# Optimization experiments

Measured on AMD Instinct MI355X. Metric: run time of the kernel, lower is better.

## Reference

```python
import jax, jax.numpy as jnp
import numpy as np

N = 50000   # nodes
E = 800000  # edges
B = 50      # graphs
EPS = 1e-5


def setup_inputs() -> dict:
    key = jax.random.key(0)
    ks = jax.random.split(key, 32)
    x = jax.random.normal(ks[0], (N, 128), dtype=jnp.float32)
    edge_index = jax.random.randint(ks[1], (2, E), 0, N, dtype=jnp.int32)
    batch = jnp.sort(jax.random.randint(ks[2], (N,), 0, B, dtype=jnp.int32))
    dims = [(128, 256), (256, 512), (512, 256), (256, 128)]
    inp = {"x": x, "edge_index": edge_index, "batch": batch}
    ki = 3
    for i, (cin, cout) in enumerate(dims, start=1):
        s = 1.0 / np.sqrt(cin)
        inp[f"conv{i}_W"] = jax.random.uniform(ks[ki], (3, cin, cout), jnp.float32, -s, s); ki += 1
        inp[f"conv{i}_b"] = jax.random.uniform(ks[ki], (cout,), jnp.float32, -s, s); ki += 1
        inp[f"gn{i}_w"] = jnp.ones((cout,), jnp.float32)
        inp[f"gn{i}_b"] = jnp.zeros((cout,), jnp.float32)
        inp[f"gn{i}_ms"] = jnp.ones((cout,), jnp.float32)
    inp["lin1_W"] = jax.random.uniform(ks[ki], (128, 64), jnp.float32, -1/np.sqrt(128), 1/np.sqrt(128)); ki += 1
    inp["lin1_b"] = jnp.zeros((64,), jnp.float32)
    inp["lin2_W"] = jax.random.uniform(ks[ki], (64, 10), jnp.float32, -1/np.sqrt(64), 1/np.sqrt(64)); ki += 1
    inp["lin2_b"] = jnp.zeros((10,), jnp.float32)
    return inp


def _cheb_conv(x, src, dst, nw, W, b):
    # PyG ChebConv, K=3, sym norm, lambda_max=2 => L_hat = -D^-1/2 A D^-1/2
    def prop(h):
        return jax.ops.segment_sum(nw[:, None] * h[src], dst, num_segments=N)
    Tx0 = x
    Tx1 = prop(x)
    Tx2 = 2.0 * prop(Tx1) - Tx0
    return Tx0 @ W[0] + Tx1 @ W[1] + Tx2 @ W[2] + b


def _graph_norm(x, batch, cnt, w, b, ms):
    mean = jax.ops.segment_sum(x, batch, num_segments=B) / cnt[:, None]
    sub = x - ms * mean[batch]
    var = jax.ops.segment_sum(sub * sub, batch, num_segments=B) / cnt[:, None]
    return w * sub * jax.lax.rsqrt(var[batch] + EPS) + b


def reference(x, edge_index, batch,
              conv1_W, conv1_b, gn1_w, gn1_b, gn1_ms,
              conv2_W, conv2_b, gn2_w, gn2_b, gn2_ms,
              conv3_W, conv3_b, gn3_w, gn3_b, gn3_ms,
              conv4_W, conv4_b, gn4_w, gn4_b, gn4_ms,
              lin1_W, lin1_b, lin2_W, lin2_b):
    src, dst = edge_index[0], edge_index[1]
    deg = jax.ops.segment_sum(jnp.ones((E,), x.dtype), dst, num_segments=N)
    dinv = jnp.where(deg > 0, jax.lax.rsqrt(jnp.maximum(deg, 1.0)), 0.0)
    nw = -dinv[src] * dinv[dst]  # scaled-Laplacian edge weights
    cnt = jnp.maximum(jax.ops.segment_sum(jnp.ones((N,), x.dtype), batch, num_segments=B), 1.0)

    h = x
    layers = [(conv1_W, conv1_b, gn1_w, gn1_b, gn1_ms),
              (conv2_W, conv2_b, gn2_w, gn2_b, gn2_ms),
              (conv3_W, conv3_b, gn3_w, gn3_b, gn3_ms),
              (conv4_W, conv4_b, gn4_w, gn4_b, gn4_ms)]
    for (W, bb, gw, gb, gms) in layers:
        h = _cheb_conv(h, src, dst, nw, W, bb)
        h = _graph_norm(h, batch, cnt, gw, gb, gms)
        h = jnp.where(h >= 0, h, 0.2 * h)  # leaky_relu(0.2)
    h = h + x  # residual
    pooled = jax.ops.segment_sum(h, batch, num_segments=B) / cnt[:, None]
    out = jnp.tanh(pooled @ lin1_W + lin1_b)
    return out @ lin2_W + lin2_b
```

## Files before the change

kernel.cpp:

```cpp
#include <hip/hip_runtime.h>

#define NN 50000
#define EE 800000
#define BG 50

typedef unsigned short ushort_t;
typedef __bf16 bf16x8 __attribute__((ext_vector_type(8)));
typedef float f32x4 __attribute__((ext_vector_type(4)));

__device__ __forceinline__ float b2f(ushort_t h) {
    unsigned int u = ((unsigned int)h) << 16;
    float f; __builtin_memcpy(&f, &u, 4); return f;
}
__device__ __forceinline__ ushort_t f2b(float f) {
    unsigned int u; __builtin_memcpy(&u, &f, 4);
    unsigned int r = u + 0x7fffu + ((u >> 16) & 1u);
    return (ushort_t)(r >> 16);
}

__device__ __forceinline__ void async_ld16(const void* g, void* l) {
    __builtin_amdgcn_global_load_lds(
        (__attribute__((address_space(1))) unsigned int*)(void*)g,
        (__attribute__((address_space(3))) unsigned int*)l, 16, 0, 0);
}

__global__ void k_detect(const ushort_t* xs, int* flag) {
    __shared__ int cnt;
    if (threadIdx.x == 0) cnt = 0;
    __syncthreads();
    int e = (xs[2 * threadIdx.x] >> 7) & 0xFF;
    if (e >= 96 && e <= 142) atomicAdd(&cnt, 1);
    __syncthreads();
    if (threadIdx.x == 0) *flag = (cnt >= 300) ? 1 : 0;
}

struct CastJobs {
    const void* src[25];
    int off[25];
    int start[26];
};
__global__ void k_castall(CastJobs jb, ushort_t* base, const int* flag, int total) {
    int i = blockIdx.x * 256 + threadIdx.x;
    if (i >= total) return;
    int lo = 0;
    while (i >= jb.start[lo + 1]) ++lo;
    int k = i - jb.start[lo];
    const void* s = jb.src[lo];
    ushort_t v;
    if (*flag) v = ((const ushort_t*)s)[k];
    else       v = f2b(((const float*)s)[k]);
    base[jb.off[lo] + k] = v;
}

__global__ void k_deg(const int* edge, int* degi) {
    int e = blockIdx.x * 256 + threadIdx.x;
    if (e < EE) atomicAdd(&degi[edge[EE + e]], 1);
}
__global__ void k_scan1(const int* degi, int* rowptr, int* bsum, float* dinv) {
    __shared__ int sh[1024];
    int t = threadIdx.x, i = blockIdx.x * 1024 + t;
    int v = (i < NN) ? degi[i] : 0;
    if (i < NN) dinv[i] = v > 0 ? rsqrtf((float)v) : 0.0f;
    sh[t] = v; __syncthreads();
    for (int off = 1; off < 1024; off <<= 1) {
        int add = (t >= off) ? sh[t - off] : 0;
        __syncthreads();
        sh[t] += add;
        __syncthreads();
    }
    if (i < NN) rowptr[i] = sh[t] - v;
    if (t == 1023) bsum[blockIdx.x] = sh[t];
}
__global__ void k_scan2(const int* bsum, int* boff, int* rowptr,
                        const int* batch, float* cntf) {
    int t = threadIdx.x;
    if (t == 0) {
        int run = 0;
        for (int j = 0; j < 49; ++j) { boff[j] = run; run += bsum[j]; }
        rowptr[NN] = run;
    }
    if (t < BG) {
        int g = t;
        int lo = 0, hi = NN;
        while (lo < hi) { int m = (lo + hi) >> 1; if (batch[m] < g) lo = m + 1; else hi = m; }
        int a = lo; lo = 0; hi = NN;
        while (lo < hi) { int m = (lo + hi) >> 1; if (batch[m] < g + 1) lo = m + 1; else hi = m; }
        cntf[g] = fmaxf((float)(lo - a), 1.0f);
    }
}
__global__ void k_scan3(int* rowptr, const int* boff) {
    int i = blockIdx.x * 256 + threadIdx.x;
    if (i < NN) rowptr[i] += boff[i >> 10];
}
__global__ void k_fill(const int* edge, const float* dinv, const int* rowptr,
                       int* cursor, int2* epack) {
    int e = blockIdx.x * 256 + threadIdx.x;
    if (e >= EE) return;
    int s = edge[e], d = edge[EE + e];
    int slot = atomicAdd(&cursor[d], 1);
    int pos = rowptr[d] + slot;
    float wv = -dinv[s] * dinv[d];
    int2 pk; pk.x = s; __builtin_memcpy(&pk.y, &wv, 4);
    epack[pos] = pk;
}

struct TJobs {
    int soff[8], doff[8], K[8], C[8];
    int tstart[9];
};
__global__ void k_transposeAll(TJobs tj, const ushort_t* Wst, ushort_t* WTall) {
    __shared__ ushort_t tile[32][33];
    int b = blockIdx.x;
    int j = 0;
    while (b >= tj.tstart[j + 1]) ++j;
    int t = b - tj.tstart[j];
    int K = tj.K[j], C = tj.C[j];
    int tilesX = K >> 5;
    int bx = (t % tilesX) * 32, by = (t / tilesX) * 32;
    const ushort_t* W = Wst + tj.soff[j];
    ushort_t* WT = WTall + tj.doff[j];
    int tx = threadIdx.x, ty = threadIdx.y;
    for (int i = ty; i < 32; i += 8) tile[i][tx] = W[(size_t)(bx + i) * C + by + tx];
    __syncthreads();
    for (int i = ty; i < 32; i += 8) WT[(size_t)(by + i) * K + bx + tx] = tile[tx][i];
}

template<int SL>
__launch_bounds__(256)
__global__ void k_prop3(ushort_t* out, int ldo,
                        const ushort_t* src, int lds_, int soff,
                        const ushort_t* addP, int lda_, int aoff,
                        const ushort_t* subP, int ldsu, int suoff,
                        const ushort_t* bias, float alpha,
                        const int* rowptr, const int2* epack) {
    constexpr int EG = 64 / SL;
    int n = blockIdx.x * 4 + (threadIdx.x >> 6);
    if (n >= NN) return;
    int lane = threadIdx.x & 63;
    int eg = lane / SL;
    int cpos = (lane % SL) * 8;
    int r0 = rowptr[n], r1 = rowptr[n + 1];
    float acc[8];
#pragma unroll
    for (int i = 0; i < 8; ++i) acc[i] = 0.f;
    const ushort_t* sbase = src + soff + cpos;
    int j = r0 + eg;
    for (; j + 7 * EG < r1; j += 8 * EG) {
        int2 p[8];
#pragma unroll
        for (int u = 0; u < 8; ++u) p[u] = epack[j + u * EG];
        __bf16 v[8][8];
#pragma unroll
        for (int u = 0; u < 8; ++u)
            __builtin_memcpy(v[u], sbase + (size_t)p[u].x * lds_, 16);
#pragma unroll
        for (int u = 0; u < 8; ++u) {
            float wv; __builtin_memcpy(&wv, &p[u].y, 4);
#pragma unroll
            for (int i = 0; i < 8; ++i) acc[i] += wv * (float)v[u][i];
        }
    }
    for (; j + 3 * EG < r1; j += 4 * EG) {
        int2 p[4];
#pragma unroll
        for (int u = 0; u < 4; ++u) p[u] = epack[j + u * EG];
        __bf16 v[4][8];
#pragma unroll
        for (int u = 0; u < 4; ++u)
            __builtin_memcpy(v[u], sbase + (size_t)p[u].x * lds_, 16);
#pragma unroll
        for (int u = 0; u < 4; ++u) {
            float wv; __builtin_memcpy(&wv, &p[u].y, 4);
#pragma unroll
            for (int i = 0; i < 8; ++i) acc[i] += wv * (float)v[u][i];
        }
    }
    for (; j < r1; j += EG) {
        int2 p0 = epack[j];
        float wv; __builtin_memcpy(&wv, &p0.y, 4);
        __bf16 v0[8];
        __builtin_memcpy(v0, sbase + (size_t)p0.x * lds_, 16);
#pragma unroll
        for (int i = 0; i < 8; ++i) acc[i] += wv * (float)v0[i];
    }
#pragma unroll
    for (int off = SL; off < 64; off <<= 1)
#pragma unroll
        for (int i = 0; i < 8; ++i) acc[i] += __shfl_xor(acc[i], off);

    if (eg == 0) {
        float res[8];
#pragma unroll
        for (int i = 0; i < 8; ++i) res[i] = alpha * acc[i];
        if (addP) {
            __bf16 a[8];
            __builtin_memcpy(a, addP + (size_t)n * lda_ + aoff + cpos, 16);
#pragma unroll
            for (int i = 0; i < 8; ++i) res[i] += (float)a[i];
        }
        if (subP) {
            __bf16 sm[8];
            __builtin_memcpy(sm, subP + (size_t)n * ldsu + suoff + cpos, 16);
#pragma unroll
            for (int i = 0; i < 8; ++i) res[i] -= (float)sm[i];
        }
        if (bias) {
            __bf16 bb[8];
            __builtin_memcpy(bb, bias + cpos, 16);
#pragma unroll
            for (int i = 0; i < 8; ++i) res[i] += (float)bb[i];
        }
        ushort_t o[8];
#pragma unroll
        for (int i = 0; i < 8; ++i) o[i] = f2b(res[i]);
        __builtin_memcpy(out + (size_t)n * ldo + cpos, o, 16);
    }
}

__launch_bounds__(256)
__global__ void k_gemm(const ushort_t* A0, const ushort_t* A1, const ushort_t* A2,
                       int lda, const ushort_t* WT, const ushort_t* bias, int hasBias,
                       ushort_t* out, int ldout, int Ktot, int NX, int MT) {
    __shared__ __align__(16) ushort_t ldsA[128 * 64];
    __shared__ __align__(16) ushort_t ldsB[128 * 64];
    const int lin = blockIdx.x;
    const int x7 = lin & 7, rr = lin >> 3;
    const int n_t = rr % NX, mhi = rr / NX;
    const int m_t = mhi * 8 + x7;
    if (m_t >= MT) return;
    const int tid = threadIdx.x, lane = tid & 63, w = tid >> 6;
    const int wm = w & 1, wn = w >> 1;
    const int m0 = m_t * 128, n0 = n_t * 128;
    const int KT = Ktot / 64, per = lda >> 6;

    f32x4 acc[4][4];
#pragma unroll
    for (int i = 0; i < 4; ++i)
#pragma unroll
        for (int j = 0; j < 4; ++j) acc[i][j] = (f32x4){0.f, 0.f, 0.f, 0.f};

    const int srow = lane >> 3;
    const int scolX = (((lane & 7) ^ srow) << 3);
    const int l7 = lane & 7;

    for (int kt = 0; kt < KT; ++kt) {
        int seg = kt / per, lk = (kt - seg * per) * 64;
        const ushort_t* Ap = (seg == 0) ? A0 : ((seg == 1) ? A1 : A2);
        __syncthreads();
#pragma unroll
        for (int t = 0; t < 4; ++t) {
            int inst = (w << 2) + t;
            int row = inst * 8 + srow;
            int gr = m0 + row; if (gr >= NN) gr = NN - 1;
            async_ld16(Ap + (size_t)gr * lda + lk + scolX, &ldsA[inst * 512]);
            async_ld16(WT + (size_t)(n0 + row) * Ktot + kt * 64 + scolX, &ldsB[inst * 512]);
        }
        __builtin_amdgcn_s_waitcnt(0);
        __syncthreads();
#pragma unroll
        for (int kk = 0; kk < 64; kk += 32) {
            bf16x8 aF[4], bF[4];
            int qx = ((((kk >> 3) + (lane >> 4)) ^ l7) << 3);
#pragma unroll
            for (int i = 0; i < 4; ++i) {
                aF[i] = *(const bf16x8*)&ldsA[(wm * 64 + i * 16 + (lane & 15)) * 64 + qx];
                bF[i] = *(const bf16x8*)&ldsB[(wn * 64 + i * 16 + (lane & 15)) * 64 + qx];
            }
#pragma unroll
            for (int i = 0; i < 4; ++i)
#pragma unroll
                for (int j = 0; j < 4; ++j)
                    acc[i][j] = __builtin_amdgcn_mfma_f32_16x16x32_bf16(aF[i], bF[j], acc[i][j], 0, 0, 0);
        }
    }
#pragma unroll
    for (int i = 0; i < 4; ++i) {
        int rbase = m0 + wm * 64 + i * 16 + ((lane >> 4) << 2);
#pragma unroll
        for (int j = 0; j < 4; ++j) {
            int col = n0 + wn * 64 + j * 16 + (lane & 15);
            float bv = hasBias ? b2f(bias[col]) : 0.0f;
#pragma unroll
            for (int r = 0; r < 4; ++r) {
                int row = rbase + r;
                if (row < NN) out[(size_t)row * ldout + col] = f2b(acc[i][j][r] + bv);
            }
        }
    }
}

template<int VEC>
__launch_bounds__(256)
__global__ void k_stats2(const ushort_t* h, const int* batch, float* sums, float* sumsq,
                         int withSq) {
    constexpr int C = VEC * 64;
    int wave = threadIdx.x >> 6, lane = threadIdx.x & 63;
    int n0 = blockIdx.x * 128 + wave * 32;
    if (n0 >= NN) return;
    int n1 = n0 + 32 < NN ? n0 + 32 : NN;
    int coff = lane * VEC;
    float s[VEC], sq[VEC];
#pragma unroll
    for (int i = 0; i < VEC; ++i) { s[i] = 0.f; sq[i] = 0.f; }
    int cur = batch[n0];
    for (int n = n0; n < n1; ++n) {
        int g = batch[n];
        if (g != cur) {
#pragma unroll
            for (int i = 0; i < VEC; ++i) {
                atomicAdd(&sums[cur * C + coff + i], s[i]);
                if (withSq) atomicAdd(&sumsq[cur * C + coff + i], sq[i]);
                s[i] = 0.f; sq[i] = 0.f;
            }
            cur = g;
        }
        __bf16 v[VEC];
        __builtin_memcpy(v, h + (size_t)n * C + coff, VEC * 2);
#pragma unroll
        for (int i = 0; i < VEC; ++i) {
            float f = (float)v[i];
            s[i] += f; sq[i] += f * f;
        }
    }
#pragma unroll
    for (int i = 0; i < VEC; ++i) {
        atomicAdd(&sums[cur * C + coff + i], s[i]);
        if (withSq) atomicAdd(&sumsq[cur * C + coff + i], sq[i]);
    }
}

template<int VEC>
__launch_bounds__(256)
__global__ void k_norm2(const ushort_t* hpre, const int* batch, const float* sums,
                        const float* sumsq, const float* cntf,
                        const ushort_t* gw, const ushort_t* gb, const ushort_t* gms,
                        const ushort_t* xres, ushort_t* out, int addres) {
    constexpr int C = VEC * 64;
    int n = blockIdx.x * 4 + (threadIdx.x >> 6);
    if (n >= NN) return;
    int lane = threadIdx.x & 63;
    int coff = lane * VEC;
    int g = batch[n];
    float cg = cntf[g];
    float sm[VEC], sq[VEC];
    __builtin_memcpy(sm, sums  + g * C + coff, VEC * 4);
    __builtin_memcpy(sq, sumsq + g * C + coff, VEC * 4);
    __bf16 vgw[VEC], vgb[VEC], vms[VEC], vh[VEC];
    __builtin_memcpy(vgw, gw + coff, VEC * 2);
    __builtin_memcpy(vgb, gb + coff, VEC * 2);
    __builtin_memcpy(vms, gms + coff, VEC * 2);
    __builtin_memcpy(vh, hpre + (size_t)n * C + coff, VEC * 2);
    __bf16 vx[VEC];
    if (addres) __builtin_memcpy(vx, xres + (size_t)n * 128 + coff, VEC * 2);
    ushort_t o[VEC];
#pragma unroll
    for (int i = 0; i < VEC; ++i) {
        float mean = sm[i] / cg;
        float ms = (float)vms[i];
        float var = sq[i] / cg - mean * mean * ms * (2.0f - ms);
        var = fmaxf(var, 0.0f);
        float y = (float)vgw[i] * ((float)vh[i] - ms * mean) * rsqrtf(var + 1e-5f) + (float)vgb[i];
        y = (y >= 0.0f) ? y : 0.2f * y;
        if (addres) y += (float)vx[i];
        o[i] = f2b(y);
    }
    __builtin_memcpy(out + (size_t)n * C + coff, o, VEC * 2);
}

__global__ void k_head(const float* pooled, const float* cntf,
                       const ushort_t* W1, const ushort_t* b1,
                       const ushort_t* W2, const ushort_t* b2s, void* out,
                       const int* flag) {
    __shared__ float pl[128];
    __shared__ float hid[64];
    int g = blockIdx.x, t = threadIdx.x;
    float inv = 1.0f / cntf[g];
    for (int k = t; k < 128; k += 64) pl[k] = pooled[g * 128 + k] * inv;
    __syncthreads();
    float a = b2f(b1[t]);
    for (int k = 0; k < 128; ++k) a += pl[k] * b2f(W1[k * 64 + t]);
    hid[t] = tanhf(a);
    __syncthreads();
    if (t < 10) {
        float o = b2f(b2s[t]);
        for (int j = 0; j < 64; ++j) o += hid[j] * b2f(W2[j * 10 + t]);
        if (*flag) ((ushort_t*)out)[g * 10 + t] = f2b(o);
        else       ((float*)out)[g * 10 + t]    = o;
    }
}

extern "C" void kernel_launch(void* const* d_in, const int* in_sizes, int n_in,
                              void* d_out, int out_size, void* d_ws, size_t ws_size,
                              hipStream_t stream) {
    (void)in_sizes; (void)n_in; (void)out_size; (void)ws_size;

    const void* x_raw = d_in[0];
    const int* edge   = (const int*)d_in[1];
    const int* batch  = (const int*)d_in[2];

    char* ws = (char*)d_ws;
    float*    dinv   = (float*)   (ws + 0);
    int*      degi   = (int*)     (ws + 200192);
    int*      rowptr = (int*)     (ws + 400384);
    int*      cursor = (int*)     (ws + 600576);
    int*      bsum   = (int*)     (ws + 800768);
    int*      boff   = (int*)     (ws + 801024);
    float*    cntf   = (float*)   (ws + 801280);
    float*    sums   = (float*)   (ws + 801536);
    float*    sumsq  = (float*)   (ws + 903936);
    float*    pooled = (float*)   (ws + 1006336);
    int*      dflag  = (int*)     (ws + 1031936);
    ushort_t* Xb     = (ushort_t*)(ws + 1032192);
    ushort_t* Wst    = (ushort_t*)(ws + 13832192);
    ushort_t* WTall  = (ushort_t*)(ws + 15798272);
    ushort_t* SB     = (ushort_t*)(ws + 17764352);
    int2*     epack  = (int2*)    (ws + 17791488);
    ushort_t* T1     = (ushort_t*)(ws + 24191488);
    ushort_t* T2     = (ushort_t*)(ws + 75391488);
    ushort_t* P      = (ushort_t*)(ws + 126591488);
    ushort_t* HA     = (ushort_t*)(ws + 177791488);

    const int cins[4]  = {128, 256, 512, 256};
    const int couts[4] = {256, 512, 256, 128};
    const size_t wtoff[4] = {0, 98304, 491520, 884736};
    const int bo[4] = {0, 256, 768, 1024};
    const int gwo = 1152, gbo = 2304, gmo = 3456;
    const int l1Wo = 4608, l1bo = 12800, l2Wo = 12864, l2bo = 13504;

    const int XB_E = 1032192 / 2, WST_E = 13832192 / 2, SB_E = 17764352 / 2;

    CastJobs jb;
    int sizes[25]; int nj = 0;
    auto addjob = [&](const void* s, int off, int n) {
        jb.src[nj] = s; jb.off[nj] = off; sizes[nj] = n; ++nj;
    };
    addjob(x_raw, XB_E, NN * 128);
    for (int l = 0; l < 4; ++l) {
        addjob(d_in[3 + 5 * l], WST_E + (int)wtoff[l], 3 * cins[l] * couts[l]);
        addjob(d_in[4 + 5 * l], SB_E + bo[l],        couts[l]);
        addjob(d_in[5 + 5 * l], SB_E + gwo + bo[l],  couts[l]);
        addjob(d_in[6 + 5 * l], SB_E + gbo + bo[l],  couts[l]);
        addjob(d_in[7 + 5 * l], SB_E + gmo + bo[l],  couts[l]);
    }
    addjob(d_in[23], SB_E + l1Wo, 128 * 64);
    addjob(d_in[24], SB_E + l1bo, 64);
    addjob(d_in[25], SB_E + l2Wo, 64 * 10);
    addjob(d_in[26], SB_E + l2bo, 10);
    int run = 0;
    for (int k = 0; k < 25; ++k) { jb.start[k] = run; run += sizes[k]; }
    jb.start[25] = run;

    TJobs tj;
    int tn = 0, trun = 0;
    auto addt = [&](int soff, int doff, int K, int C) {
        tj.soff[tn] = soff; tj.doff[tn] = doff; tj.K[tn] = K; tj.C[tn] = C;
        tj.tstart[tn] = trun; trun += (K / 32) * (C / 32); ++tn;
    };
    addt((int)wtoff[0], (int)wtoff[0], 3 * cins[0], couts[0]);
    addt((int)wtoff[1], (int)wtoff[1], 3 * cins[1], couts[1]);
    for (int l = 2; l < 4; ++l)
        for (int j2 = 0; j2 < 3; ++j2) {
            int o = (int)wtoff[l] + j2 * cins[l] * couts[l];
            addt(o, o, cins[l], couts[l]);
        }
    tj.tstart[8] = trun;

    k_detect<<<1, 512, 0, stream>>>((const ushort_t*)x_raw, dflag);
    hipMemsetAsync(degi,   0, NN * 4, stream);
    hipMemsetAsync(cursor, 0, NN * 4, stream);
    hipMemsetAsync(pooled, 0, BG * 128 * 4, stream);

    k_castall<<<(run + 255) / 256, 256, 0, stream>>>(jb, (ushort_t*)ws, dflag, run);

    k_deg<<<(EE + 255) / 256, 256, 0, stream>>>(edge, degi);
    k_scan1<<<49, 1024, 0, stream>>>(degi, rowptr, bsum, dinv);
    k_scan2<<<1, 64, 0, stream>>>(bsum, boff, rowptr, batch, cntf);
    k_scan3<<<(NN + 255) / 256, 256, 0, stream>>>(rowptr, boff);
    k_fill<<<(EE + 255) / 256, 256, 0, stream>>>(edge, dinv, rowptr, cursor, epack);

    k_transposeAll<<<trun, dim3(32, 8), 0, stream>>>(tj, Wst, WTall);

    const int NB = (NN + 3) / 4;
    const int SBk = (NN + 127) / 128;
    const int MT = (NN + 127) / 128;
    const int MG = (MT + 7) / 8;
    auto prop = [&](int C, ushort_t* o, int ldo,
                    const ushort_t* s, int lds_, int soff,
                    const ushort_t* aP, int lda_, int aoff,
                    const ushort_t* sP, int ldsu, int suoff,
                    const ushort_t* bias, float alpha) {
        if (C == 128)
            k_prop3<16><<<NB, 256, 0, stream>>>(o, ldo, s, lds_, soff, aP, lda_, aoff,
                                                sP, ldsu, suoff, bias, alpha, rowptr, epack);
        else
            k_prop3<32><<<NB, 256, 0, stream>>>(o, ldo, s, lds_, soff, aP, lda_, aoff,
                                                sP, ldsu, suoff, bias, alpha, rowptr, epack);
    };
    auto gemm = [&](const ushort_t* A0, const ushort_t* A1, const ushort_t* A2,
                    int lda, const ushort_t* WT, const ushort_t* bias, int hasBias,
                    ushort_t* o, int ldout, int Ktot, int NX) {
        k_gemm<<<MG * 8 * NX, 256, 0, stream>>>(A0, A1, A2, lda, WT, bias, hasBias,
                                                o, ldout, Ktot, NX, MT);
    };
    auto stats = [&](int C, const ushort_t* h, float* sm, float* sq, int withSq) {
        if (C == 128)      k_stats2<2><<<SBk, 256, 0, stream>>>(h, batch, sm, sq, withSq);
        else if (C == 256) k_stats2<4><<<SBk, 256, 0, stream>>>(h, batch, sm, sq, withSq);
        else               k_stats2<8><<<SBk, 256, 0, stream>>>(h, batch, sm, sq, withSq);
    };
    auto norm = [&](int C, const ushort_t* hp, const ushort_t* gwp, const ushort_t* gbp,
                    const ushort_t* gmp, ushort_t* o, int addres) {
        if (C == 128)      k_norm2<2><<<NB, 256, 0, stream>>>(hp, batch, sums, sumsq, cntf, gwp, gbp, gmp, Xb, o, addres);
        else if (C == 256) k_norm2<4><<<NB, 256, 0, stream>>>(hp, batch, sums, sumsq, cntf, gwp, gbp, gmp, Xb, o, addres);
        else               k_norm2<8><<<NB, 256, 0, stream>>>(hp, batch, sums, sumsq, cntf, gwp, gbp, gmp, Xb, o, addres);
    };

    ushort_t* G = T1;
    const ushort_t* hin = Xb;
    for (int l = 0; l < 4; ++l) {
        int cin = cins[l], cout = couts[l];
        if (l < 2) {
            prop(cin, T1, cin, hin, cin, 0, nullptr, 0, 0, nullptr, 0, 0, nullptr, 1.0f);
            prop(cin, T2, cin, T1, cin, 0, nullptr, 0, 0, hin, cin, 0, nullptr, 2.0f);
            gemm(hin, T1, T2, cin, WTall + wtoff[l], SB + bo[l], 1, P, cout, 3 * cin,
                 cout / 128);
        } else {
            gemm(hin, hin, hin, cin, WTall + wtoff[l], nullptr, 0, G, 3 * cout, cin,
                 (3 * cout) / 128);
            ushort_t* V = HA;
            prop(cout, V, cout, G, 3 * cout, 2 * cout, G, 3 * cout, cout,
                 nullptr, 0, 0, nullptr, 2.0f);
            prop(cout, P, cout, V, cout, 0, G, 3 * cout, 0,
                 G, 3 * cout, 2 * cout, SB + bo[l], 1.0f);
        }
        hipMemsetAsync(sums, 0, 2 * 102400, stream);
        stats(cout, P, sums, sumsq, 1);
        norm(cout, P, SB + gwo + bo[l], SB + gbo + bo[l], SB + gmo + bo[l], HA, l == 3);
        hin = HA;
    }
    stats(128, HA, pooled, pooled, 0);
    k_head<<<BG, 64, 0, stream>>>(pooled, cntf, SB + l1Wo, SB + l1bo, SB + l2Wo, SB + l2bo,
                                  d_out, dflag);
}
```

Baseline: 1.109 ms.

## Compute graph stats per-graph block without atomics and drop memsets

Result: slower. 1.275 ms (+15.0%).

```diff
diff --git a/kernel.cpp b/kernel.cpp
--- a/kernel.cpp
+++ b/kernel.cpp
@@ -39,8 +39,10 @@
     int off[25];
     int start[26];
 };
-__global__ void k_castall(CastJobs jb, ushort_t* base, const int* flag, int total) {
+__global__ void k_castall(CastJobs jb, ushort_t* base, const int* flag, int total,
+                          int* degi) {
     int i = blockIdx.x * 256 + threadIdx.x;
+    if (i < NN) degi[i] = 0;
     if (i >= total) return;
     int lo = 0;
     while (i >= jb.start[lo + 1]) ++lo;
@@ -72,12 +74,13 @@
     if (t == 1023) bsum[blockIdx.x] = sh[t];
 }
 __global__ void k_scan2(const int* bsum, int* boff, int* rowptr,
-                        const int* batch, float* cntf) {
+                        const int* batch, float* cntf, int* gstart) {
     int t = threadIdx.x;
     if (t == 0) {
         int run = 0;
         for (int j = 0; j < 49; ++j) { boff[j] = run; run += bsum[j]; }
         rowptr[NN] = run;
+        gstart[BG] = NN;
     }
     if (t < BG) {
         int g = t;
@@ -85,12 +88,13 @@
         while (lo < hi) { int m = (lo + hi) >> 1; if (batch[m] < g) lo = m + 1; else hi = m; }
         int a = lo; lo = 0; hi = NN;
         while (lo < hi) { int m = (lo + hi) >> 1; if (batch[m] < g + 1) lo = m + 1; else hi = m; }
+        gstart[g] = a;
         cntf[g] = fmaxf((float)(lo - a), 1.0f);
     }
 }
-__global__ void k_scan3(int* rowptr, const int* boff) {
+__global__ void k_scan3(int* rowptr, const int* boff, int* cursor) {
     int i = blockIdx.x * 256 + threadIdx.x;
-    if (i < NN) rowptr[i] += boff[i >> 10];
+    if (i < NN) { rowptr[i] += boff[i >> 10]; cursor[i] = 0; }
 }
 __global__ void k_fill(const int* edge, const float* dinv, const int* rowptr,
                        int* cursor, int2* epack) {
@@ -145,21 +149,6 @@
     for (int i = 0; i < 8; ++i) acc[i] = 0.f;
     const ushort_t* sbase = src + soff + cpos;
     int j = r0 + eg;
-    for (; j + 7 * EG < r1; j += 8 * EG) {
-        int2 p[8];
-#pragma unroll
-        for (int u = 0; u < 8; ++u) p[u] = epack[j + u * EG];
-        __bf16 v[8][8];
-#pragma unroll
-        for (int u = 0; u < 8; ++u)
-            __builtin_memcpy(v[u], sbase + (size_t)p[u].x * lds_, 16);
-#pragma unroll
-        for (int u = 0; u < 8; ++u) {
-            float wv; __builtin_memcpy(&wv, &p[u].y, 4);
-#pragma unroll
-            for (int i = 0; i < 8; ++i) acc[i] += wv * (float)v[u][i];
-        }
-    }
     for (; j + 3 * EG < r1; j += 4 * EG) {
         int2 p[4];
 #pragma unroll
@@ -291,29 +280,18 @@
 
 template<int VEC>
 __launch_bounds__(256)
-__global__ void k_stats2(const ushort_t* h, const int* batch, float* sums, float* sumsq,
-                         int withSq) {
+__global__ void k_stats3(const ushort_t* h, const int* gstart,
+                         float* sums, float* sumsq, int withSq) {
     constexpr int C = VEC * 64;
+    __shared__ float ls[4][C], lq[4][C];
+    int g = blockIdx.x;
+    int gs = gstart[g], ge = gstart[g + 1];
     int wave = threadIdx.x >> 6, lane = threadIdx.x & 63;
-    int n0 = blockIdx.x * 128 + wave * 32;
-    if (n0 >= NN) return;
-    int n1 = n0 + 32 < NN ? n0 + 32 : NN;
     int coff = lane * VEC;
     float s[VEC], sq[VEC];
 #pragma unroll
     for (int i = 0; i < VEC; ++i) { s[i] = 0.f; sq[i] = 0.f; }
-    int cur = batch[n0];
-    for (int n = n0; n < n1; ++n) {
-        int g = batch[n];
-        if (g != cur) {
-#pragma unroll
-            for (int i = 0; i < VEC; ++i) {
-                atomicAdd(&sums[cur * C + coff + i], s[i]);
-                if (withSq) atomicAdd(&sumsq[cur * C + coff + i], sq[i]);
-                s[i] = 0.f; sq[i] = 0.f;
-            }
-            cur = g;
-        }
+    for (int n = gs + wave; n < ge; n += 4) {
         __bf16 v[VEC];
         __builtin_memcpy(v, h + (size_t)n * C + coff, VEC * 2);
 #pragma unroll
@@ -323,9 +301,19 @@
         }
     }
 #pragma unroll
-    for (int i = 0; i < VEC; ++i) {
-        atomicAdd(&sums[cur * C + coff + i], s[i]);
-        if (withSq) atomicAdd(&sumsq[cur * C + coff + i], sq[i]);
+    for (int i = 0; i < VEC; ++i) { ls[wave][coff + i] = s[i]; lq[wave][coff + i] = sq[i]; }
+    __syncthreads();
+    if (wave == 0) {
+#pragma unroll
+        for (int i = 0; i < VEC; ++i) {
+            int c = coff + i;
+            float ts = ls[0][c] + ls[1][c] + ls[2][c] + ls[3][c];
+            sums[g * C + c] = ts;
+            if (withSq) {
+                float tq = lq[0][c] + lq[1][c] + lq[2][c] + lq[3][c];
+                sumsq[g * C + c] = tq;
+            }
+        }
     }
 }
 
@@ -406,10 +394,11 @@
     int*      bsum   = (int*)     (ws + 800768);
     int*      boff   = (int*)     (ws + 801024);
     float*    cntf   = (float*)   (ws + 801280);
-    float*    sums   = (float*)   (ws + 801536);
-    float*    sumsq  = (float*)   (ws + 903936);
-    float*    pooled = (float*)   (ws + 1006336);
-    int*      dflag  = (int*)     (ws + 1031936);
+    int*      dflag  = (int*)     (ws + 801488);
+    int*      gstart = (int*)     (ws + 801536);
+    float*    sums   = (float*)   (ws + 801792);
+    float*    sumsq  = (float*)   (ws + 904192);
+    float*    pooled = (float*)   (ws + 1006592);
     ushort_t* Xb     = (ushort_t*)(ws + 1032192);
     ushort_t* Wst    = (ushort_t*)(ws + 13832192);
     ushort_t* WTall  = (ushort_t*)(ws + 15798272);
@@ -466,22 +455,17 @@
     tj.tstart[8] = trun;
 
     k_detect<<<1, 512, 0, stream>>>((const ushort_t*)x_raw, dflag);
-    hipMemsetAsync(degi,   0, NN * 4, stream);
-    hipMemsetAsync(cursor, 0, NN * 4, stream);
-    hipMemsetAsync(pooled, 0, BG * 128 * 4, stream);
-
-    k_castall<<<(run + 255) / 256, 256, 0, stream>>>(jb, (ushort_t*)ws, dflag, run);
+    k_castall<<<(run + 255) / 256, 256, 0, stream>>>(jb, (ushort_t*)ws, dflag, run, degi);
 
     k_deg<<<(EE + 255) / 256, 256, 0, stream>>>(edge, degi);
     k_scan1<<<49, 1024, 0, stream>>>(degi, rowptr, bsum, dinv);
-    k_scan2<<<1, 64, 0, stream>>>(bsum, boff, rowptr, batch, cntf);
-    k_scan3<<<(NN + 255) / 256, 256, 0, stream>>>(rowptr, boff);
+    k_scan2<<<1, 64, 0, stream>>>(bsum, boff, rowptr, batch, cntf, gstart);
+    k_scan3<<<(NN + 255) / 256, 256, 0, stream>>>(rowptr, boff, cursor);
     k_fill<<<(EE + 255) / 256, 256, 0, stream>>>(edge, dinv, rowptr, cursor, epack);
 
     k_transposeAll<<<trun, dim3(32, 8), 0, stream>>>(tj, Wst, WTall);
 
     const int NB = (NN + 3) / 4;
-    const int SBk = (NN + 127) / 128;
     const int MT = (NN + 127) / 128;
     const int MG = (MT + 7) / 8;
     auto prop = [&](int C, ushort_t* o, int ldo,
@@ -503,9 +487,9 @@
                                                 o, ldout, Ktot, NX, MT);
     };
     auto stats = [&](int C, const ushort_t* h, float* sm, float* sq, int withSq) {
-        if (C == 128)      k_stats2<2><<<SBk, 256, 0, stream>>>(h, batch, sm, sq, withSq);
-        else if (C == 256) k_stats2<4><<<SBk, 256, 0, stream>>>(h, batch, sm, sq, withSq);
-        else               k_stats2<8><<<SBk, 256, 0, stream>>>(h, batch, sm, sq, withSq);
+        if (C == 128)      k_stats3<2><<<BG, 256, 0, stream>>>(h, gstart, sm, sq, withSq);
+        else if (C == 256) k_stats3<4><<<BG, 256, 0, stream>>>(h, gstart, sm, sq, withSq);
+        else               k_stats3<8><<<BG, 256, 0, stream>>>(h, gstart, sm, sq, withSq);
     };
     auto norm = [&](int C, const ushort_t* hp, const ushort_t* gwp, const ushort_t* gbp,
                     const ushort_t* gmp, ushort_t* o, int addres) {
@@ -532,7 +516,6 @@
             prop(cout, P, cout, V, cout, 0, G, 3 * cout, 0,
                  G, 3 * cout, 2 * cout, SB + bo[l], 1.0f);
         }
-        hipMemsetAsync(sums, 0, 2 * 102400, stream);
         stats(cout, P, sums, sumsq, 1);
         norm(cout, P, SB + gwo + bo[l], SB + gbo + bo[l], SB + gmo + bo[l], HA, l == 3);
         hin = HA;
```
